# Optimization experiments

Hardware: AMD Instinct MI355X
Metric: run time of the kernel (lower is better)

Reference implementation:

```python
import jax, jax.numpy as jnp
import numpy as np

B, C, H, W = 16, 96, 96, 96
K, N, R, CR = 4, 8, 6, 12  # scan dirs, d_state, dt_rank, SE hidden


def channel_ln(x, g, b, eps=1e-6):
    # LayerNorm over channel dim (channel_first)
    mu = jnp.mean(x, axis=1, keepdims=True)
    var = jnp.var(x, axis=1, keepdims=True)
    return (x - mu) * jax.lax.rsqrt(var + eps) * g[None, :, None, None] + b[None, :, None, None]


def conv1x1(x, w, b):
    return jnp.einsum('bchw,dc->bdhw', x, w) + b[None, :, None, None]


def ss2d(x, xproj_w, dtproj_w, dtproj_b, A_logs, Ds, g, bta):
    # 4-direction selective scan (VMamba SS2D core). x: (B,C,H,W)
    Bq, Cq, Hq, Wq = x.shape
    L = Hq * Wq
    xf = x.reshape(Bq, Cq, L)
    xt = jnp.transpose(x, (0, 1, 3, 2)).reshape(Bq, Cq, L)
    xs = jnp.stack([xf, xt, xf[..., ::-1], xt[..., ::-1]], axis=1)  # (B,K,C,L)
    x_dbl = jnp.einsum('bkcl,kdc->bkdl', xs, xproj_w)  # (B,K,R+2N,L)
    dts, Bs, Cs = jnp.split(x_dbl, [R, R + N], axis=2)
    delta = jax.nn.softplus(jnp.einsum('bkrl,kcr->bkcl', dts, dtproj_w) + dtproj_b[None, :, :, None])
    A = -jnp.exp(A_logs)  # (K,C,N)
    u_t = jnp.moveaxis(xs, -1, 0)   # (L,B,K,C)
    d_t = jnp.moveaxis(delta, -1, 0)
    B_t = jnp.moveaxis(Bs, -1, 0)   # (L,B,K,N)
    C_t = jnp.moveaxis(Cs, -1, 0)
    h0 = jnp.zeros((Bq, K, Cq, N), x.dtype)

    @jax.checkpoint
    def step(h, inp):
        u, d, Bv, Cv = inp
        dA = jnp.exp(d[..., None] * A)                      # (B,K,C,N)
        h = dA * h + (d * u)[..., None] * Bv[:, :, None, :]
        return h, jnp.sum(h * Cv[:, :, None, :], axis=-1)   # (B,K,C)

    _, ys = jax.lax.scan(step, h0, (u_t, d_t, B_t, C_t))
    ys = jnp.moveaxis(ys, 0, -1) + Ds[None, :, :, None] * xs  # (B,K,C,L)

    def untrans(yk):
        return jnp.transpose(yk.reshape(Bq, Cq, Wq, Hq), (0, 1, 3, 2)).reshape(Bq, Cq, L)

    out = ys[:, 0] + untrans(ys[:, 1]) + ys[:, 2, :, ::-1] + untrans(ys[:, 3][..., ::-1])
    return channel_ln(out.reshape(Bq, Cq, Hq, Wq), g, bta)


def block_forward(x, ln_g, ln_b, p1_w, p1_b, p2in_w, p2in_b, dw_w, dw_b,
                  xproj_w, dtproj_w, dtproj_b, A_logs, Ds, ssln_g, ssln_b,
                  p2n_g, p2n_b, ca_w1, ca_b1, ca_w2, ca_b2, block_idx):
    h = channel_ln(x, ln_g, ln_b)
    a = jax.nn.silu(conv1x1(h, p1_w, p1_b))
    z = conv1x1(h, p2in_w, p2in_b)
    z = jax.lax.conv_general_dilated(z, dw_w, (1, 1), 'SAME',
                                     dimension_numbers=('NCHW', 'OIHW', 'NCHW'),
                                     feature_group_count=z.shape[1]) + dw_b[None, :, None, None]
    z = jax.nn.silu(z)
    if block_idx % 2 == 0:
        z = jnp.transpose(z, (0, 1, 3, 2))
    else:
        z = z[:, :, ::-1, ::-1]
    z = ss2d(z, xproj_w, dtproj_w, dtproj_b, A_logs, Ds, ssln_g, ssln_b)
    if block_idx % 2 == 0:
        z = jnp.transpose(z, (0, 1, 3, 2))
    else:
        z = z[:, :, ::-1, ::-1]
    z = channel_ln(z, p2n_g, p2n_b)
    y = a * z
    # channel attention (SE)
    s = jnp.mean(y, axis=(2, 3))  # (B,C)
    att = jax.nn.sigmoid(jnp.einsum('cr,br->bc', ca_w2,
                                    jax.nn.silu(jnp.einsum('rc,bc->br', ca_w1, s) + ca_b1)) + ca_b2)
    return x + y * att[:, :, None, None]


def local_mamba(x, params, block_idx):
    b, c, h, w = x.shape
    h2, w2 = h // 2, w // 2
    qs = jnp.stack([x[:, :, :h2, :w2], x[:, :, :h2, w2:],
                    x[:, :, h2:, :w2], x[:, :, h2:, w2:]])  # (4,B,C,h2,w2)
    fn = lambda q, *p: block_forward(q, *p, block_idx)
    outs = jax.vmap(fn)(qs, *params)
    top = jnp.concatenate([outs[0], outs[1]], axis=3)
    bot = jnp.concatenate([outs[2], outs[3]], axis=3)
    return jnp.concatenate([top, bot], axis=2)


def setup_inputs() -> dict:
    key = jax.random.key(0)
    ks = jax.random.split(key, 12)
    rn = lambda k, shape, s=1.0: jax.random.normal(k, shape, jnp.float32) * s
    return dict(
        x=rn(ks[0], (B, C, H, W)),
        ln_g=jnp.ones((4, C)), ln_b=jnp.zeros((4, C)),
        p1_w=rn(ks[1], (4, C, C), C ** -0.5), p1_b=jnp.zeros((4, C)),
        p2in_w=rn(ks[2], (4, C, C), C ** -0.5), p2in_b=jnp.zeros((4, C)),
        dw_w=rn(ks[3], (4, C, 1, 3, 3), 1.0 / 3.0), dw_b=jnp.zeros((4, C)),
        xproj_w=rn(ks[4], (4, K, R + 2 * N, C), C ** -0.5),
        dtproj_w=rn(ks[5], (4, K, C, R), R ** -0.5),
        dtproj_b=rn(ks[6], (4, K, C), 0.1),
        A_logs=jax.random.uniform(ks[7], (4, K, C, N), jnp.float32, 0.0, 1.0),
        Ds=jnp.ones((4, K, C)),
        ssln_g=jnp.ones((4, C)), ssln_b=jnp.zeros((4, C)),
        p2n_g=jnp.ones((4, C)), p2n_b=jnp.zeros((4, C)),
        ca_w1=rn(ks[8], (4, CR, C), C ** -0.5), ca_b1=jnp.zeros((4, CR)),
        ca_w2=rn(ks[9], (4, C, CR), CR ** -0.5), ca_b2=jnp.zeros((4, C)),
        block_idx=0,
    )


def reference(x, ln_g, ln_b, p1_w, p1_b, p2in_w, p2in_b, dw_w, dw_b,
              xproj_w, dtproj_w, dtproj_b, A_logs, Ds, ssln_g, ssln_b,
              p2n_g, p2n_b, ca_w1, ca_b1, ca_w2, ca_b2, block_idx):
    params = (ln_g, ln_b, p1_w, p1_b, p2in_w, p2in_b, dw_w, dw_b,
              xproj_w, dtproj_w, dtproj_b, A_logs, Ds, ssln_g, ssln_b,
              p2n_g, p2n_b, ca_w1, ca_b1, ca_w2, ca_b2)
    return local_mamba(x, params, block_idx)
```

## Files before the change

kernel.cpp:

```cpp
#include <hip/hip_runtime.h>
#include <hip/hip_bf16.h>

#define BQ 16
#define CN 96
#define HQ 48
#define LL 2304
#define NK 4
#define RR 6
#define NNS 8
#define DPJ 22
#define CRr 12
#define LOG2E 1.4426950408889634f

using bf16 = __hip_bfloat16;

typedef __attribute__((ext_vector_type(8))) short bf16x8;
typedef __attribute__((ext_vector_type(4))) float f32x4;

__device__ __forceinline__ float b2f(bf16 v) { return __bfloat162float(v); }
__device__ __forceinline__ bf16  f2b(float v){ return __float2bfloat16(v); }
__device__ __forceinline__ float bflo(unsigned u){ return __uint_as_float(u << 16); }
__device__ __forceinline__ float bfhi(unsigned u){ return __uint_as_float(u & 0xffff0000u); }
__device__ __forceinline__ float sigf(float x){ return 1.f / (1.f + __expf(-x)); }
__device__ __forceinline__ float siluf(float x){ return x / (1.f + __expf(-x)); }
__device__ __forceinline__ unsigned packbf(float a, float b){
    unsigned lo = (unsigned)__builtin_bit_cast(unsigned short, f2b(a));
    unsigned hi = (unsigned)__builtin_bit_cast(unsigned short, f2b(b));
    return lo | (hi << 16);
}
__device__ __forceinline__ unsigned rot16(unsigned u){ return (u >> 16) | (u << 16); }
__device__ __forceinline__ void unpack8(uint4 v, float* f){
    f[0]=bflo(v.x); f[1]=bfhi(v.x); f[2]=bflo(v.y); f[3]=bfhi(v.y);
    f[4]=bflo(v.z); f[5]=bfhi(v.z); f[6]=bflo(v.w); f[7]=bfhi(v.w);
}
__device__ __forceinline__ void unpack4(uint2 v, float* f){
    f[0]=bflo(v.x); f[1]=bfhi(v.x); f[2]=bflo(v.y); f[3]=bfhi(v.y);
}
__device__ __forceinline__ float fexp2(float x){
#if __has_builtin(__builtin_amdgcn_exp2f)
    return __builtin_amdgcn_exp2f(x);
#else
    return __expf(x * 0.6931471805599453f);
#endif
}
__device__ __forceinline__ float qxor(float v, int ctrl_b1){
    int x;
    if (ctrl_b1) x = __builtin_amdgcn_mov_dpp(__float_as_int(v), 0xB1, 0xF, 0xF, true);
    else         x = __builtin_amdgcn_mov_dpp(__float_as_int(v), 0x4E, 0xF, 0xF, true);
    return __int_as_float(x);
}

__global__ __launch_bounds__(192) void k_lnconv(
    const float* __restrict__ x, const float* __restrict__ ln_g, const float* __restrict__ ln_b,
    const float* __restrict__ p1w, const float* __restrict__ p1b,
    const float* __restrict__ p2w, const float* __restrict__ p2b,
    bf16* __restrict__ a_out, bf16* __restrict__ z0_out)
{
    const int hh2 = blockIdx.x;
    const int b = blockIdx.y, q = blockIdx.z;
    const int h0 = (q >> 1) * HQ, w0 = (q & 1) * HQ;
    const int tid = threadIdx.x;
    const int qb = q * BQ + b;

    __shared__ alignas(16) bf16 wl2[192 * 104];
    __shared__ alignas(16) bf16 hn2[96 * 104];
    __shared__ float mu[96], rs[96];
    __shared__ float pmu[192], pv2[192];
    __shared__ float biasLds[192];
    __shared__ float gl[96], bl[96];

    for (int t = tid; t < 192 * 24; t += 192) {
        int row = t / 24, c4 = (t % 24) * 4;
        const float* srcw = (row < 96) ? &p1w[(q * CN + row) * CN + c4]
                                       : &p2w[(q * CN + (row - 96)) * CN + c4];
        float4 wv = *reinterpret_cast<const float4*>(srcw);
        uint2 pk; pk.x = packbf(wv.x, wv.y); pk.y = packbf(wv.z, wv.w);
        *reinterpret_cast<uint2*>(&wl2[row * 104 + c4]) = pk;
    }
    if (tid < 192)
        biasLds[tid] = (tid < 96) ? p1b[q * CN + tid] : p2b[q * CN + (tid - 96)];
    if (tid < 96) { gl[tid] = ln_g[q * CN + tid]; bl[tid] = ln_b[q * CN + tid]; }
    for (int t = tid; t < CN * 24; t += 192) {
        int c = t / 24, v = t % 24;
        int row = v / 12, col = (v % 12) * 4;
        int p = row * 48 + col;
        float4 xv = *reinterpret_cast<const float4*>(
            &x[((b * CN + c) * 96 + h0 + 2 * hh2 + row) * 96 + w0 + col]);
        hn2[p * 104 + c]       = f2b(xv.x);
        hn2[(p + 1) * 104 + c] = f2b(xv.y);
        hn2[(p + 2) * 104 + c] = f2b(xv.z);
        hn2[(p + 3) * 104 + c] = f2b(xv.w);
    }
    __syncthreads();
    {
        int p = tid % 96, half = tid / 96;
        const bf16* hp = &hn2[p * 104 + half * 48];
        float s = 0.f, s2 = 0.f;
        #pragma unroll
        for (int c8 = 0; c8 < 48; c8 += 8) {
            float f[8]; unpack8(*reinterpret_cast<const uint4*>(hp + c8), f);
            #pragma unroll
            for (int i = 0; i < 8; ++i) { s += f[i]; s2 += f[i] * f[i]; }
        }
        pmu[half * 96 + p] = s; pv2[half * 96 + p] = s2;
    }
    __syncthreads();
    if (tid < 96) {
        float s = pmu[tid] + pmu[96 + tid];
        float s2 = pv2[tid] + pv2[96 + tid];
        float m = s * (1.f / 96.f);
        float var = s2 * (1.f / 96.f) - m * m;
        mu[tid] = m; rs[tid] = rsqrtf(var + 1e-6f);
    }
    __syncthreads();
    for (int t = tid; t < 96 * 12; t += 192) {
        int p = t / 12, c8 = (t % 12) * 8;
        float f[8]; unpack8(*reinterpret_cast<const uint4*>(&hn2[p * 104 + c8]), f);
        float m = mu[p], r = rs[p];
        unsigned ou[4];
        #pragma unroll
        for (int i = 0; i < 8; i += 2) {
            float v0 = (f[i]     - m) * r * gl[c8 + i]     + bl[c8 + i];
            float v1 = (f[i + 1] - m) * r * gl[c8 + i + 1] + bl[c8 + i + 1];
            ou[i >> 1] = packbf(v0, v1);
        }
        uint4 ov; ov.x = ou[0]; ov.y = ou[1]; ov.z = ou[2]; ov.w = ou[3];
        *reinterpret_cast<uint4*>(&hn2[p * 104 + c8]) = ov;
    }
    __syncthreads();
    const int w = tid >> 6;
    const int l = tid & 63;
    const int lr = l & 15;
    const int lq = l >> 4;
    f32x4 acc[4][6];
    #pragma unroll
    for (int m = 0; m < 4; ++m)
        #pragma unroll
        for (int n = 0; n < 6; ++n)
            acc[m][n] = (f32x4){0.f, 0.f, 0.f, 0.f};
    #pragma unroll
    for (int k0 = 0; k0 < 96; k0 += 32) {
        bf16x8 afr[4], bfr[6];
        #pragma unroll
        for (int m = 0; m < 4; ++m)
            afr[m] = *reinterpret_cast<const bf16x8*>(
                &wl2[(w * 64 + m * 16 + lr) * 104 + k0 + lq * 8]);
        #pragma unroll
        for (int n = 0; n < 6; ++n)
            bfr[n] = *reinterpret_cast<const bf16x8*>(
                &hn2[(n * 16 + lr) * 104 + k0 + lq * 8]);
        #pragma unroll
        for (int m = 0; m < 4; ++m)
            #pragma unroll
            for (int n = 0; n < 6; ++n)
                acc[m][n] = __builtin_amdgcn_mfma_f32_16x16x32_bf16(
                    afr[m], bfr[n], acc[m][n], 0, 0, 0);
    }
    #pragma unroll
    for (int m = 0; m < 4; ++m) {
        const int Rbase = w * 64 + m * 16 + lq * 4;
        #pragma unroll
        for (int n = 0; n < 6; ++n) {
            const int col = n * 16 + lr;
            const int colin = (col >= 48) ? (col - 48) : col;
            const int lbase = (2 * hh2 + (col >= 48 ? 1 : 0)) * 48 + colin;
            #pragma unroll
            for (int r = 0; r < 4; ++r) {
                const int R = Rbase + r;
                const bool isA = R < 96;
                const int d = isA ? R : R - 96;
                float v = acc[m][n][r] + biasLds[R];
                if (isA) v = siluf(v);
                bf16* dst = isA ? a_out : z0_out;
                dst[(size_t)(qb * CN + d) * LL + lbase] = f2b(v);
            }
        }
    }
}

__global__ __launch_bounds__(256) void k_dwconv(
    const bf16* __restrict__ z0, const float* __restrict__ dww, const float* __restrict__ dwb,
    const int* __restrict__ bidx, bf16* __restrict__ zt, bf16* __restrict__ ztT)
{
    const int c = blockIdx.x, b = blockIdx.y, q = blockIdx.z;
    const int tid = threadIdx.x;
    const int base = ((q * BQ + b) * CN + c) * LL;
    __shared__ float zin[50 * 50];
    __shared__ float zo[48 * 49];
    if (tid < 196) {
        int idx;
        if (tid < 50)       idx = tid;
        else if (tid < 100) idx = 49 * 50 + (tid - 50);
        else if (tid < 148) idx = (tid - 99) * 50;
        else                idx = (tid - 147) * 50 + 49;
        zin[idx] = 0.f;
    }
    for (int t = tid; t < 288; t += 256) {
        uint4 v = *reinterpret_cast<const uint4*>(&z0[base + t * 8]);
        float f[8]; unpack8(v, f);
        int e0 = t * 8, row = e0 / 48, col = e0 % 48;
        float* dst = &zin[(row + 1) * 50 + col + 1];
        #pragma unroll
        for (int i = 0; i < 8; ++i) dst[i] = f[i];
    }
    float wk[9];
    #pragma unroll
    for (int i = 0; i < 9; ++i) wk[i] = dww[(q * CN + c) * 9 + i];
    const float bias = dwb[q * CN + c];
    __syncthreads();
    for (int t = tid; t < LL; t += 256) {
        int hh = t / 48, ww = t % 48;
        const float* z0r = &zin[hh * 50 + ww];
        float s = bias;
        s = fmaf(wk[0], z0r[0],        s);
        s = fmaf(wk[1], z0r[1],        s);
        s = fmaf(wk[2], z0r[2],        s);
        s = fmaf(wk[3], z0r[50],       s);
        s = fmaf(wk[4], z0r[51],       s);
        s = fmaf(wk[5], z0r[52],       s);
        s = fmaf(wk[6], z0r[100],      s);
        s = fmaf(wk[7], z0r[101],      s);
        s = fmaf(wk[8], z0r[102],      s);
        zo[hh * 49 + ww] = siluf(s);
    }
    __syncthreads();
    const bool even = ((bidx[0] & 1) == 0);
    for (int idx = tid; idx < 288; idx += 256) {
        int e0 = idx * 8, i = e0 / 48, j = e0 % 48;
        float vz[8], vzT[8];
        if (even) {
            #pragma unroll
            for (int m = 0; m < 8; ++m) { vz[m] = zo[(j + m) * 49 + i];  vzT[m] = zo[i * 49 + j + m]; }
        } else {
            #pragma unroll
            for (int m = 0; m < 8; ++m) { vz[m] = zo[(47 - i) * 49 + (47 - j - m)];
                                          vzT[m] = zo[(47 - j - m) * 49 + (47 - i)]; }
        }
        uint4 oa, ob;
        oa.x = packbf(vz[0], vz[1]);   oa.y = packbf(vz[2], vz[3]);
        oa.z = packbf(vz[4], vz[5]);   oa.w = packbf(vz[6], vz[7]);
        ob.x = packbf(vzT[0], vzT[1]); ob.y = packbf(vzT[2], vzT[3]);
        ob.z = packbf(vzT[4], vzT[5]); ob.w = packbf(vzT[6], vzT[7]);
        *reinterpret_cast<uint4*>(&zt[base + e0])  = oa;
        *reinterpret_cast<uint4*>(&ztT[base + e0]) = ob;
    }
}

__global__ __launch_bounds__(192) void k_xdbl(
    const bf16* __restrict__ zt, const bf16* __restrict__ ztT,
    const float* __restrict__ xprojw, bf16* __restrict__ xdbl)
{
    const int lt = blockIdx.x, k = blockIdx.y, qb = blockIdx.z;
    const int tid = threadIdx.x;
    const int l0 = lt * 96;
    const int q = qb >> 4;
    __shared__ alignas(16) bf16 wl3[32 * 104];
    __shared__ alignas(16) bf16 tmp[96 * 104];
    __shared__ alignas(16) bf16 ub[96 * 104];
    const bf16* __restrict__ src = (k & 1) ? ztT : zt;
    const bool rev = (k >= 2);

    for (int t = tid; t < 520; t += 192)
        reinterpret_cast<unsigned*>(&wl3[22 * 104])[t] = 0u;
    for (int t = tid; t < DPJ * 24; t += 192) {
        int d = t / 24, c4 = (t % 24) * 4;
        float4 wv = *reinterpret_cast<const float4*>(
            &xprojw[((q * NK + k) * DPJ + d) * CN + c4]);
        uint2 pk; pk.x = packbf(wv.x, wv.y); pk.y = packbf(wv.z, wv.w);
        *reinterpret_cast<uint2*>(&wl3[d * 104 + c4]) = pk;
    }
    for (int t = tid; t < CN * 12; t += 192) {
        int cc = t / 12, j0 = (t % 12) * 8;
        uint4 v;
        if (!rev) {
            v = *reinterpret_cast<const uint4*>(&src[(size_t)(qb * CN + cc) * LL + l0 + j0]);
        } else {
            v = *reinterpret_cast<const uint4*>(&src[(size_t)(qb * CN + cc) * LL + (LL - (l0 + j0) - 8)]);
            uint4 r; r.x = rot16(v.w); r.y = rot16(v.z); r.z = rot16(v.y); r.w = rot16(v.x);
            v = r;
        }
        *reinterpret_cast<uint4*>(&tmp[cc * 104 + j0]) = v;
    }
    __syncthreads();
    for (int t = tid; t < 96 * 12; t += 192) {
        int ll = t % 96, c0 = (t / 96) * 8;
        const unsigned short* ts = reinterpret_cast<const unsigned short*>(tmp);
        unsigned e[8];
        #pragma unroll
        for (int i = 0; i < 8; ++i) e[i] = ts[(c0 + i) * 104 + ll];
        uint4 v;
        v.x = e[0] | (e[1] << 16); v.y = e[2] | (e[3] << 16);
        v.z = e[4] | (e[5] << 16); v.w = e[6] | (e[7] << 16);
        *reinterpret_cast<uint4*>(&ub[ll * 104 + c0]) = v;
    }
    __syncthreads();
    const int w = tid >> 6;
    const int ln = tid & 63;
    const int lr = ln & 15;
    const int lq = ln >> 4;
    f32x4 acc[2][2];
    #pragma unroll
    for (int m = 0; m < 2; ++m)
        #pragma unroll
        for (int n = 0; n < 2; ++n)
            acc[m][n] = (f32x4){0.f, 0.f, 0.f, 0.f};
    #pragma unroll
    for (int k0 = 0; k0 < 96; k0 += 32) {
        bf16x8 afr[2], bfr[2];
        #pragma unroll
        for (int m = 0; m < 2; ++m)
            afr[m] = *reinterpret_cast<const bf16x8*>(
                &wl3[(m * 16 + lr) * 104 + k0 + lq * 8]);
        #pragma unroll
        for (int n = 0; n < 2; ++n)
            bfr[n] = *reinterpret_cast<const bf16x8*>(
                &ub[((2 * w + n) * 16 + lr) * 104 + k0 + lq * 8]);
        #pragma unroll
        for (int m = 0; m < 2; ++m)
            #pragma unroll
            for (int n = 0; n < 2; ++n)
                acc[m][n] = __builtin_amdgcn_mfma_f32_16x16x32_bf16(
                    afr[m], bfr[n], acc[m][n], 0, 0, 0);
    }
    const size_t obase = (size_t)(qb * NK + k) * (DPJ * LL);
    #pragma unroll
    for (int m = 0; m < 2; ++m) {
        #pragma unroll
        for (int n = 0; n < 2; ++n) {
            const int lpos = l0 + (2 * w + n) * 16 + lr;
            #pragma unroll
            for (int r = 0; r < 4; ++r) {
                const int d = m * 16 + lq * 4 + r;
                if (d < DPJ)
                    xdbl[obase + (size_t)d * LL + lpos] = f2b(acc[m][n][r]);
            }
        }
    }
}


#define SCAN_BARRIER() asm volatile("s_waitcnt lgkmcnt(0)\n\ts_barrier" ::: "memory")

#define UWORD(NUA, IDX) (((IDX) & 3) == 0 ? NUA[(IDX) >> 2].x : \
                         ((IDX) & 3) == 1 ? NUA[(IDX) >> 2].y : \
                         ((IDX) & 3) == 2 ? NUA[(IDX) >> 2].z : NUA[(IDX) >> 2].w)

#define ROT3(v) (v) = ((v) == 2) ? 0 : ((v) + 1)

__global__ __launch_bounds__(384) void k_scan(
    const bf16* __restrict__ zt, const bf16* __restrict__ ztT,
    const bf16* __restrict__ xdbl,
    const float* __restrict__ dtw_g, const float* __restrict__ dtb_g,
    const float* __restrict__ Alog_g, const float* __restrict__ Ds_g,
    bf16* __restrict__ ys)
{
    const int bid = blockIdx.x;
    const int ch2 = bid & 1, k = (bid >> 1) & 3, qb = bid >> 3, q = qb >> 4;
    const int qk = q * NK + k;
    const int tid = threadIdx.x;
    const bool isScan = (tid < 192);
    const int lt = isScan ? tid : (tid - 192);
    const int ca = lt >> 2, p = lt & 3;
    const int c = ch2 * 48 + ca;

    __shared__ float dd3[3][48 * 52];
    __shared__ float xr3[3][6 * 52];
    __shared__ float bcv3[3][48 * 16];

    const bf16* __restrict__ src = (k & 1) ? ztT : zt;
    const bool rev = (k >= 2);
    const int ja = p * 12;

    float wdt[6] = {0.f, 0.f, 0.f, 0.f, 0.f, 0.f};
    float dtbc = 0.f;
    if (!isScan) {
        const float* wp = dtw_g + (size_t)qk * CN * RR + c * RR;
        float2 wa = *reinterpret_cast<const float2*>(wp);
        float2 wb = *reinterpret_cast<const float2*>(wp + 2);
        float2 wc = *reinterpret_cast<const float2*>(wp + 4);
        wdt[0] = wa.x; wdt[1] = wa.y; wdt[2] = wb.x; wdt[3] = wb.y; wdt[4] = wc.x; wdt[5] = wc.y;
        dtbc = dtb_g[qk * CN + c];
    }
    const bool xload = (!isScan) && (lt < 132);
    const int vr = lt / 6, jx = (lt % 6) * 8;
    const bf16* gx = xdbl + (size_t)(qb * NK + k) * (DPJ * LL) + (size_t)vr * LL + jx;
    int bccol = 0;
    if (vr >= 6) {
        int v = vr - 6;
        int n = v & 7;
        bccol = (n >> 1) * 4 + ((v >= 8) ? 2 : 0) + (n & 1);
    }

    float A0L = 0.f, A1L = 0.f, Dc = 0.f;
    if (isScan) {
        A0L = -__expf(Alog_g[((size_t)qk * CN + c) * NNS + 2 * p])     * LOG2E;
        A1L = -__expf(Alog_g[((size_t)qk * CN + c) * NNS + 2 * p + 1]) * LOG2E;
        Dc = Ds_g[qk * CN + c];
    }
    float h0 = 0.f, h1 = 0.f;
    const bf16* gu = src + (size_t)(qb * CN + c) * LL + (rev ? (LL - 48) : 0);
    const int ustep = rev ? -48 : 48;
    bf16* yp = ys + (size_t)(qb * NK + k) * (CN * LL) + (size_t)c * LL;

    #define COMMIT_BLOCK(PXV, XRB, BCB) do {                                          \
        if (xload) {                                                                  \
            float g[8]; unpack8(PXV, g);                                              \
            if (vr < 6) {                                                             \
                *reinterpret_cast<float4*>(&(XRB)[vr * 52 + jx])                      \
                    = make_float4(g[0], g[1], g[2], g[3]);                            \
                *reinterpret_cast<float4*>(&(XRB)[vr * 52 + jx + 4])                  \
                    = make_float4(g[4], g[5], g[6], g[7]);                            \
            } else {                                                                  \
                _Pragma("unroll")                                                     \
                for (int i = 0; i < 8; ++i) (BCB)[(jx + i) * 16 + bccol] = g[i];      \
            }                                                                         \
        }                                                                             \
    } while (0)

    #define DELTA_BLOCK(XRB, DDB) do {                                                \
        float acc[12];                                                                \
        _Pragma("unroll")                                                             \
        for (int i = 0; i < 12; ++i) acc[i] = dtbc;                                   \
        _Pragma("unroll")                                                             \
        for (int r = 0; r < 6; ++r) {                                                 \
            float4 d0 = *reinterpret_cast<const float4*>(&(XRB)[r * 52 + ja]);        \
            float4 d1 = *reinterpret_cast<const float4*>(&(XRB)[r * 52 + ja + 4]);    \
            float4 d2 = *reinterpret_cast<const float4*>(&(XRB)[r * 52 + ja + 8]);    \
            float wr_ = wdt[r];                                                       \
            acc[0] = fmaf(wr_, d0.x, acc[0]);  acc[1] = fmaf(wr_, d0.y, acc[1]);      \
            acc[2] = fmaf(wr_, d0.z, acc[2]);  acc[3] = fmaf(wr_, d0.w, acc[3]);      \
            acc[4] = fmaf(wr_, d1.x, acc[4]);  acc[5] = fmaf(wr_, d1.y, acc[5]);      \
            acc[6] = fmaf(wr_, d1.z, acc[6]);  acc[7] = fmaf(wr_, d1.w, acc[7]);      \
            acc[8] = fmaf(wr_, d2.x, acc[8]);  acc[9] = fmaf(wr_, d2.y, acc[9]);      \
            acc[10] = fmaf(wr_, d2.z, acc[10]); acc[11] = fmaf(wr_, d2.w, acc[11]);   \
        }                                                                             \
        _Pragma("unroll")                                                             \
        for (int i = 0; i < 12; ++i) {                                                \
            float a = acc[i];                                                         \
            acc[i] = (a > 15.f) ? a : __logf(1.f + __expf(a));                        \
        }                                                                             \
        float4* dp = reinterpret_cast<float4*>(&(DDB)[ca * 52 + ja]);                 \
        dp[0] = make_float4(acc[0], acc[1], acc[2], acc[3]);                          \
        dp[1] = make_float4(acc[4], acc[5], acc[6], acc[7]);                          \
        dp[2] = make_float4(acc[8], acc[9], acc[10], acc[11]);                        \
    } while (0)

    uint4 u_a[6], u_b[6];
    uint4 px_a = {0,0,0,0}, px_b = {0,0,0,0}, px1 = {0,0,0,0};
    if (isScan) {
        #pragma unroll
        for (int i = 0; i < 6; ++i) u_a[i] = *reinterpret_cast<const uint4*>(gu + i * 8);
        gu += ustep;
        #pragma unroll
        for (int i = 0; i < 6; ++i) u_b[i] = *reinterpret_cast<const uint4*>(gu + i * 8);
        gu += ustep;
    } else {
        uint4 px0 = {0,0,0,0};
        if (xload) {
            px0  = *reinterpret_cast<const uint4*>(gx);
            px1  = *reinterpret_cast<const uint4*>(gx + 48);
            px_a = *reinterpret_cast<const uint4*>(gx + 96);
            px_b = *reinterpret_cast<const uint4*>(gx + 144);
            gx += 192;
        }
        COMMIT_BLOCK(px0, xr3[0], bcv3[0]);
    }
    SCAN_BARRIER();
    if (!isScan) {
        DELTA_BLOCK(xr3[0], dd3[0]);
        COMMIT_BLOCK(px1, xr3[1], bcv3[1]);
    }
    SCAN_BARRIER();

    int s_cur = 0;
    int d_idx = 1, c_idx = 2;

    #define PROD_BODY(CH, PX) do {                                                    \
        const int chp_ = (CH);                                                        \
        if (chp_ + 2 < 48) COMMIT_BLOCK(PX, xr3[c_idx], bcv3[c_idx]);                 \
        if (chp_ + 4 < 48 && xload) { PX = *reinterpret_cast<const uint4*>(gx); gx += 48; } \
        if (chp_ + 1 < 48) DELTA_BLOCK(xr3[d_idx], dd3[d_idx]);                       \
        ROT3(d_idx); ROT3(c_idx);                                                     \
    } while (0)

    #define SCAN_CHUNK(CH, UC) do {                                                   \
        const int ch_ = (CH);                                                         \
        uint4 nu[6];                                                                  \
        if (!rev) {                                                                   \
            nu[0] = UC[0]; nu[1] = UC[1]; nu[2] = UC[2];                              \
            nu[3] = UC[3]; nu[4] = UC[4]; nu[5] = UC[5];                              \
        } else {                                                                      \
            _Pragma("unroll")                                                         \
            for (int qq = 0; qq < 6; ++qq) {                                          \
                nu[qq].x = rot16(UC[5 - qq].w); nu[qq].y = rot16(UC[5 - qq].z);       \
                nu[qq].z = rot16(UC[5 - qq].y); nu[qq].w = rot16(UC[5 - qq].x);       \
            }                                                                         \
        }                                                                             \
        {                                                                             \
            const int l0 = ch_ * 48;                                                  \
            const float* ddc = &dd3[s_cur][ca * 52];                                  \
            const float* bcc = &bcv3[s_cur][p * 4];                                   \
            _Pragma("unroll")                                                         \
            for (int gg = 0; gg < 6; ++gg) {                                          \
                unsigned pk[4];                                                       \
                _Pragma("unroll")                                                     \
                for (int half = 0; half < 2; ++half) {                                \
                    const int j0 = gg * 8 + half * 4;                                 \
                    float4 d4 = *reinterpret_cast<const float4*>(ddc + j0);           \
                    const float* df = reinterpret_cast<const float*>(&d4);            \
                    _Pragma("unroll")                                                 \
                    for (int s = 0; s < 4; ++s) {                                     \
                        const int j = j0 + s;                                         \
                        const unsigned uwv = UWORD(nu, j >> 1);                       \
                        float u = (j & 1) ? bfhi(uwv) : bflo(uwv);                    \
                        float d = df[s];                                              \
                        float4 bq = *reinterpret_cast<const float4*>(bcc + j * 16);   \
                        float du = d * u;                                             \
                        float dA0 = fexp2(d * A0L);                                   \
                        float dA1 = fexp2(d * A1L);                                   \
                        h0 = fmaf(dA0, h0, du * bq.x);                                \
                        h1 = fmaf(dA1, h1, du * bq.y);                                \
                        float y = fmaf(h0, bq.z, h1 * bq.w);                          \
                        y += qxor(y, 1); y += qxor(y, 0);                             \
                        y = fmaf(Dc, u, y);                                           \
                        unsigned hb = (unsigned)__builtin_bit_cast(unsigned short, f2b(y)); \
                        const int sl = half * 4 + s;                                  \
                        if (sl & 1) pk[sl >> 1] |= hb << 16; else pk[sl >> 1] = hb;   \
                    }                                                                 \
                }                                                                     \
                if (p == 0) {                                                         \
                    uint4 wv4; wv4.x = pk[0]; wv4.y = pk[1]; wv4.z = pk[2]; wv4.w = pk[3]; \
                    *reinterpret_cast<uint4*>(yp + l0 + gg * 8) = wv4;                \
                }                                                                     \
            }                                                                         \
        }                                                                             \
        if (ch_ + 2 < 48) {                                                           \
            _Pragma("unroll")                                                         \
            for (int i = 0; i < 6; ++i) UC[i] = *reinterpret_cast<const uint4*>(gu + i * 8); \
            gu += ustep;                                                              \
        }                                                                             \
        ROT3(s_cur);                                                                  \
    } while (0)

    for (int t = 0; t < 24; ++t) {
        if (isScan) SCAN_CHUNK(2 * t, u_a);
        else        PROD_BODY(2 * t, px_a);
        SCAN_BARRIER();
        if (isScan) SCAN_CHUNK(2 * t + 1, u_b);
        else        PROD_BODY(2 * t + 1, px_b);
        SCAN_BARRIER();
    }

    #undef SCAN_CHUNK
    #undef PROD_BODY
    #undef DELTA_BLOCK
    #undef COMMIT_BLOCK
}

__global__ __launch_bounds__(256) void k_sum(
    const bf16* __restrict__ ys, bf16* __restrict__ s_out)
{
    const int c = blockIdx.x, b = blockIdx.y, q = blockIdx.z;
    const int qb = q * BQ + b;
    const int tid = threadIdx.x;
    __shared__ float t0[48 * 49];
    __shared__ float t2[48 * 49];
    const size_t base0 = ((size_t)(qb * NK + 0) * CN + c) * LL;
    const size_t base1 = ((size_t)(qb * NK + 1) * CN + c) * LL;
    const size_t base2 = ((size_t)(qb * NK + 2) * CN + c) * LL;
    const size_t base3 = ((size_t)(qb * NK + 3) * CN + c) * LL;
    for (int idx = tid; idx < 288; idx += 256) {
        int e0 = idx * 8, h = e0 / 48, w = e0 % 48;
        float f[8];
        unpack8(*reinterpret_cast<const uint4*>(&ys[base0 + e0]), f);
        #pragma unroll
        for (int i = 0; i < 8; ++i) t0[h * 49 + w + i] = f[i];
        unpack8(*reinterpret_cast<const uint4*>(&ys[base2 + e0]), f);
        #pragma unroll
        for (int i = 0; i < 8; ++i) t2[h * 49 + w + i] = f[i];
    }
    __syncthreads();
    const size_t cbase = ((size_t)qb * CN + c) * LL;
    for (int idx = tid; idx < 288; idx += 256) {
        int m0 = idx * 8, ww = m0 / 48, hh = m0 % 48;
        float f1[8], f3[8];
        unpack8(*reinterpret_cast<const uint4*>(&ys[base1 + m0]), f1);
        unpack8(*reinterpret_cast<const uint4*>(&ys[base3 + (LL - 8 - m0)]), f3);
        float o[8];
        #pragma unroll
        for (int i = 0; i < 8; ++i) {
            float v0 = t0[(hh + i) * 49 + ww];
            float v2 = t2[(47 - hh - i) * 49 + (47 - ww)];
            o[i] = v0 + f1[i] + v2 + f3[7 - i];
        }
        uint4 w;
        w.x = packbf(o[0], o[1]); w.y = packbf(o[2], o[3]);
        w.z = packbf(o[4], o[5]); w.w = packbf(o[6], o[7]);
        *reinterpret_cast<uint4*>(&s_out[cbase + m0]) = w;
    }
}

__global__ __launch_bounds__(256) void k_combine(
    const bf16* __restrict__ s_in, const bf16* __restrict__ a_in,
    const float* __restrict__ ssg, const float* __restrict__ ssb,
    const float* __restrict__ png, const float* __restrict__ pnb,
    const int* __restrict__ bidx,
    bf16* __restrict__ y_out, float* __restrict__ s_buf)
{
    const int ww = blockIdx.x, b = blockIdx.y, q = blockIdx.z;
    const int qb = q * BQ + b;
    const int tid = threadIdx.x;
    __shared__ float o[CN * 48];
    __shared__ float mu[48], rs[48];
    __shared__ float pp[192], pp2[192];
    for (int v = tid; v < 576; v += 256) {
        int e0 = v * 8, cc = e0 / 48, hh = e0 % 48;
        float f[8];
        unpack8(*reinterpret_cast<const uint4*>(&s_in[((size_t)qb * CN + cc) * LL + ww * 48 + hh]), f);
        #pragma unroll
        for (int i = 0; i < 8; ++i) o[cc * 48 + hh + i] = f[i];
    }
    __syncthreads();
    if (tid < 192) {
        int hh = tid % 48, part = tid / 48;
        float s = 0.f, s2 = 0.f;
        int c0 = part * 24;
        for (int cc = c0; cc < c0 + 24; ++cc) { float v = o[cc * 48 + hh]; s += v; s2 += v * v; }
        pp[tid] = s; pp2[tid] = s2;
    }
    __syncthreads();
    if (tid < 48) {
        float s = pp[tid] + pp[tid + 48] + pp[tid + 96] + pp[tid + 144];
        float s2 = pp2[tid] + pp2[tid + 48] + pp2[tid + 96] + pp2[tid + 144];
        float m = s * (1.f / 96.f), var = s2 * (1.f / 96.f) - m * m;
        mu[tid] = m; rs[tid] = rsqrtf(var + 1e-6f);
    }
    __syncthreads();
    for (int t = tid; t < CN * 48; t += 256) {
        int cc = t / 48, hh = t % 48;
        o[t] = (o[t] - mu[hh]) * rs[hh] * ssg[q * CN + cc] + ssb[q * CN + cc];
    }
    __syncthreads();
    if (tid < 192) {
        int hh = tid % 48, part = tid / 48;
        float s = 0.f, s2 = 0.f;
        int c0 = part * 24;
        for (int cc = c0; cc < c0 + 24; ++cc) { float v = o[cc * 48 + hh]; s += v; s2 += v * v; }
        pp[tid] = s; pp2[tid] = s2;
    }
    __syncthreads();
    if (tid < 48) {
        float s = pp[tid] + pp[tid + 48] + pp[tid + 96] + pp[tid + 144];
        float s2 = pp2[tid] + pp2[tid + 48] + pp2[tid + 96] + pp2[tid + 144];
        float m = s * (1.f / 96.f), var = s2 * (1.f / 96.f) - m * m;
        mu[tid] = m; rs[tid] = rsqrtf(var + 1e-6f);
    }
    __syncthreads();
    const bool even = ((bidx[0] & 1) == 0);
    if (even) {
        for (int v = tid; v < 576; v += 256) {
            int e0 = v * 8, cc = e0 / 48, hh = e0 % 48;
            size_t oidx = ((size_t)qb * CN + cc) * LL + ww * 48 + hh;
            float af[8];
            unpack8(*reinterpret_cast<const uint4*>(&a_in[oidx]), af);
            float yv[8];
            #pragma unroll
            for (int i = 0; i < 8; ++i) {
                float z2 = (o[cc * 48 + hh + i] - mu[hh + i]) * rs[hh + i] * png[q * CN + cc] + pnb[q * CN + cc];
                yv[i] = af[i] * z2;
                o[cc * 48 + hh + i] = yv[i];
            }
            uint4 w;
            w.x = packbf(yv[0], yv[1]); w.y = packbf(yv[2], yv[3]);
            w.z = packbf(yv[4], yv[5]); w.w = packbf(yv[6], yv[7]);
            *reinterpret_cast<uint4*>(&y_out[oidx]) = w;
        }
    } else {
        for (int t = tid; t < CN * 48; t += 256) {
            int cc = t / 48, hh = t % 48;
            float z2 = (o[t] - mu[hh]) * rs[hh] * png[q * CN + cc] + pnb[q * CN + cc];
            size_t oidx = ((size_t)qb * CN + cc) * LL + (47 - hh) * 48 + (47 - ww);
            float yv = b2f(a_in[oidx]) * z2;
            y_out[oidx] = f2b(yv);
            o[t] = yv;
        }
    }
    __syncthreads();
    if (tid < CN) {
        float s = 0.f;
        for (int j = 0; j < 48; ++j) s += o[tid * 48 + j];
        atomicAdd(&s_buf[qb * CN + tid], s);
    }
}

__global__ __launch_bounds__(256) void k_final(
    const float* __restrict__ x, const bf16* __restrict__ y_in,
    const float* __restrict__ s_buf,
    const float* __restrict__ w1, const float* __restrict__ b1,
    const float* __restrict__ w2, const float* __restrict__ b2,
    float* __restrict__ out)
{
    const int c = blockIdx.x, b = blockIdx.y, q = blockIdx.z;
    const int h0 = (q >> 1) * HQ, w0 = (q & 1) * HQ;
    const int qb = q * BQ + b;
    const int tid = threadIdx.x;
    __shared__ float tl[CRr];
    __shared__ float tpart[16 * CRr];
    __shared__ float attv;
    if (tid < 192) {
        int r = tid % CRr, part = tid / CRr;
        float acc = 0.f;
        const float* wr = w1 + (q * CRr + r) * CN;
        const float* sb = s_buf + qb * CN;
        int c0 = part * 6;
        for (int cc = c0; cc < c0 + 6; ++cc)
            acc = fmaf(wr[cc], sb[cc] * (1.f / (float)LL), acc);
        tpart[part * CRr + r] = acc;
    }
    __syncthreads();
    if (tid < CRr) {
        float acc = b1[q * CRr + tid];
        #pragma unroll
        for (int pt = 0; pt < 16; ++pt) acc += tpart[pt * CRr + tid];
        tl[tid] = siluf(acc);
    }
    __syncthreads();
    if (tid == 0) {
        float acc = b2[q * CN + c];
        #pragma unroll
        for (int r = 0; r < CRr; ++r) acc = fmaf(w2[(q * CN + c) * CRr + r], tl[r], acc);
        attv = sigf(acc);
    }
    __syncthreads();
    const float av = attv;
    const size_t ybase = (size_t)(qb * CN + c) * LL;
    const int xb = (b * CN + c) * 9216 + h0 * 96 + w0;
    for (int t = tid; t < LL / 8; t += 256) {
        int e0 = t * 8;
        int gi = xb + (e0 / 48) * 96 + (e0 % 48);
        uint4 yv = *reinterpret_cast<const uint4*>(&y_in[ybase + e0]);
        float yf[8]; unpack8(yv, yf);
        float4 xa = *reinterpret_cast<const float4*>(&x[gi]);
        float4 xc = *reinterpret_cast<const float4*>(&x[gi + 4]);
        float4 o0 = {xa.x + yf[0]*av, xa.y + yf[1]*av, xa.z + yf[2]*av, xa.w + yf[3]*av};
        float4 o1 = {xc.x + yf[4]*av, xc.y + yf[5]*av, xc.z + yf[6]*av, xc.w + yf[7]*av};
        *reinterpret_cast<float4*>(&out[gi])     = o0;
        *reinterpret_cast<float4*>(&out[gi + 4]) = o1;
    }
}

extern "C" void kernel_launch(void* const* d_in, const int* in_sizes, int n_in,
                              void* d_out, int out_size, void* d_ws, size_t ws_size,
                              hipStream_t stream)
{
    (void)in_sizes; (void)n_in; (void)out_size; (void)ws_size;
    const float* x       = (const float*)d_in[0];
    const float* ln_g    = (const float*)d_in[1];
    const float* ln_b    = (const float*)d_in[2];
    const float* p1_w    = (const float*)d_in[3];
    const float* p1_b    = (const float*)d_in[4];
    const float* p2in_w  = (const float*)d_in[5];
    const float* p2in_b  = (const float*)d_in[6];
    const float* dw_w    = (const float*)d_in[7];
    const float* dw_b    = (const float*)d_in[8];
    const float* xproj_w = (const float*)d_in[9];
    const float* dtproj_w= (const float*)d_in[10];
    const float* dtproj_b= (const float*)d_in[11];
    const float* A_logs  = (const float*)d_in[12];
    const float* Ds      = (const float*)d_in[13];
    const float* ssln_g  = (const float*)d_in[14];
    const float* ssln_b  = (const float*)d_in[15];
    const float* p2n_g   = (const float*)d_in[16];
    const float* p2n_b   = (const float*)d_in[17];
    const float* ca_w1   = (const float*)d_in[18];
    const float* ca_b1   = (const float*)d_in[19];
    const float* ca_w2   = (const float*)d_in[20];
    const float* ca_b2   = (const float*)d_in[21];
    const int*  bidx     = (const int*)d_in[22];
    float* out = (float*)d_out;

    char* ws = (char*)d_ws;
    const size_t off_a    = 0;
    const size_t off_zt   = 28311552;
    const size_t off_ztT  = 56623104;
    const size_t off_xdbl = 84934656;
    const size_t off_ys   = 110886912;
    const size_t off_z0   = off_ys;
    const size_t off_s    = off_zt;
    const size_t off_y    = off_ztT;
    const size_t off_sb   = 224133120;

    bf16*  a_buf   = (bf16*)(ws + off_a);
    bf16*  zt_buf  = (bf16*)(ws + off_zt);
    bf16*  ztT_buf = (bf16*)(ws + off_ztT);
    bf16*  xdbl_buf= (bf16*)(ws + off_xdbl);
    bf16*  ys_buf  = (bf16*)(ws + off_ys);
    bf16*  z0_buf  = (bf16*)(ws + off_z0);
    bf16*  s_sum   = (bf16*)(ws + off_s);
    bf16*  y_buf   = (bf16*)(ws + off_y);
    float* s_buf   = (float*)(ws + off_sb);

    (void)hipMemsetAsync(ws + off_sb, 0, 24576, stream);

    k_lnconv<<<dim3(24, 16, 4), 192, 0, stream>>>(
        x, ln_g, ln_b, p1_w, p1_b, p2in_w, p2in_b, a_buf, z0_buf);
    k_dwconv<<<dim3(96, 16, 4), 256, 0, stream>>>(
        z0_buf, dw_w, dw_b, bidx, zt_buf, ztT_buf);
    k_xdbl<<<dim3(24, 4, 64), 192, 0, stream>>>(
        zt_buf, ztT_buf, xproj_w, xdbl_buf);
    k_scan<<<dim3(512), 384, 0, stream>>>(
        zt_buf, ztT_buf, xdbl_buf, dtproj_w, dtproj_b, A_logs, Ds, ys_buf);
    k_sum<<<dim3(96, 16, 4), 256, 0, stream>>>(
        ys_buf, s_sum);
    k_combine<<<dim3(48, 16, 4), 256, 0, stream>>>(
        s_sum, a_buf, ssln_g, ssln_b, p2n_g, p2n_b, bidx, y_buf, s_buf);
    k_final<<<dim3(96, 16, 4), 256, 0, stream>>>(
        x, y_buf, s_buf, ca_w1, ca_b1, ca_w2, ca_b2, out);
}
```

Measured before the change: 604.8 us.

## Split selective scan into segmented three-pass scan with carry propagation

Replaces the single sequential scan kernel with a chunked parallel scan. The first pass computes per-segment state and decay products over 12 segments. A small kernel prefix-combines the carries, and the final pass rescans each segment from its carried-in state and writes outputs. This exposes far more blocks than the original 512-block launch to hide the serial-latency bound. In exchange it reads the inputs twice, recomputes delta and exp in both passes, and needs extra workspace, so it falls back to the old kernel when the workspace is too small.

```diff
diff --git a/kernel.cpp b/kernel.cpp
--- a/kernel.cpp
+++ b/kernel.cpp
@@ -212,15 +212,15 @@
         int hh = t / 48, ww = t % 48;
         const float* z0r = &zin[hh * 50 + ww];
         float s = bias;
-        s = fmaf(wk[0], z0r[0],        s);
-        s = fmaf(wk[1], z0r[1],        s);
-        s = fmaf(wk[2], z0r[2],        s);
-        s = fmaf(wk[3], z0r[50],       s);
-        s = fmaf(wk[4], z0r[51],       s);
-        s = fmaf(wk[5], z0r[52],       s);
-        s = fmaf(wk[6], z0r[100],      s);
-        s = fmaf(wk[7], z0r[101],      s);
-        s = fmaf(wk[8], z0r[102],      s);
+        s = fmaf(wk[0], z0r[0],   s);
+        s = fmaf(wk[1], z0r[1],   s);
+        s = fmaf(wk[2], z0r[2],   s);
+        s = fmaf(wk[3], z0r[50],  s);
+        s = fmaf(wk[4], z0r[51],  s);
+        s = fmaf(wk[5], z0r[52],  s);
+        s = fmaf(wk[6], z0r[100], s);
+        s = fmaf(wk[7], z0r[101], s);
+        s = fmaf(wk[8], z0r[102], s);
         zo[hh * 49 + ww] = siluf(s);
     }
     __syncthreads();
@@ -557,6 +557,310 @@
     #undef COMMIT_BLOCK
 }
 
+#define SEGCH 4
+#define NSEG 12
+
+__global__ __launch_bounds__(192) void k_scanA(
+    const bf16* __restrict__ zt, const bf16* __restrict__ ztT,
+    const bf16* __restrict__ xdbl,
+    const float* __restrict__ dtw_g, const float* __restrict__ dtb_g,
+    const float* __restrict__ Alog_g,
+    float4* __restrict__ carry)
+{
+    const int bid = blockIdx.x;
+    const int seg = bid % NSEG, rest = bid / NSEG;
+    const int ch2 = rest & 1, k = (rest >> 1) & 3, qb = rest >> 3, q = qb >> 4;
+    const int qk = q * NK + k;
+    const int lt = threadIdx.x;
+    const int ca = lt >> 2, p = lt & 3;
+    const int c = ch2 * 48 + ca;
+
+    __shared__ float dd[48 * 52];
+    __shared__ float xr[6 * 52];
+    __shared__ float bcv[48 * 16];
+
+    const float* wp = dtw_g + (size_t)qk * CN * RR + c * RR;
+    float wdt[6];
+    {
+        float2 wa = *reinterpret_cast<const float2*>(wp);
+        float2 wb = *reinterpret_cast<const float2*>(wp + 2);
+        float2 wc = *reinterpret_cast<const float2*>(wp + 4);
+        wdt[0] = wa.x; wdt[1] = wa.y; wdt[2] = wb.x; wdt[3] = wb.y; wdt[4] = wc.x; wdt[5] = wc.y;
+    }
+    const float dtbc = dtb_g[qk * CN + c];
+    const float A0L = -__expf(Alog_g[((size_t)qk * CN + c) * NNS + 2 * p])     * LOG2E;
+    const float A1L = -__expf(Alog_g[((size_t)qk * CN + c) * NNS + 2 * p + 1]) * LOG2E;
+    const bf16* __restrict__ src = (k & 1) ? ztT : zt;
+    const bool rev = (k >= 2);
+    const int ja = p * 12;
+    const bool xload = (lt < 132);
+    const int vr = lt / 6, jx = (lt % 6) * 8;
+    int bccol = 0;
+    if (vr >= 6) {
+        int v = vr - 6;
+        int n = v & 7;
+        bccol = (n >> 1) * 4 + ((v >= 8) ? 2 : 0) + (n & 1);
+    }
+    const size_t xb = (size_t)(qb * NK + k) * (DPJ * LL);
+    const size_t ubase = (size_t)(qb * CN + c) * LL;
+
+    float h0 = 0.f, h1 = 0.f, a0 = 1.f, a1 = 1.f;
+
+    for (int ch = 0; ch < SEGCH; ++ch) {
+        const int g = seg * SEGCH + ch;
+        uint4 uu[6];
+        {
+            const bf16* gu = src + ubase + (rev ? (LL - 48 - 48 * g) : 48 * g);
+            #pragma unroll
+            for (int i = 0; i < 6; ++i) uu[i] = *reinterpret_cast<const uint4*>(gu + i * 8);
+        }
+        uint4 px = {0,0,0,0};
+        if (xload) px = *reinterpret_cast<const uint4*>(&xdbl[xb + (size_t)vr * LL + g * 48 + jx]);
+        __syncthreads();
+        if (xload) {
+            float gv[8]; unpack8(px, gv);
+            if (vr < 6) {
+                *reinterpret_cast<float4*>(&xr[vr * 52 + jx])     = make_float4(gv[0], gv[1], gv[2], gv[3]);
+                *reinterpret_cast<float4*>(&xr[vr * 52 + jx + 4]) = make_float4(gv[4], gv[5], gv[6], gv[7]);
+            } else {
+                #pragma unroll
+                for (int i = 0; i < 8; ++i) bcv[(jx + i) * 16 + bccol] = gv[i];
+            }
+        }
+        __syncthreads();
+        {
+            float acc[12];
+            #pragma unroll
+            for (int i = 0; i < 12; ++i) acc[i] = dtbc;
+            #pragma unroll
+            for (int r = 0; r < 6; ++r) {
+                float4 d0 = *reinterpret_cast<const float4*>(&xr[r * 52 + ja]);
+                float4 d1 = *reinterpret_cast<const float4*>(&xr[r * 52 + ja + 4]);
+                float4 d2 = *reinterpret_cast<const float4*>(&xr[r * 52 + ja + 8]);
+                float wr_ = wdt[r];
+                acc[0] = fmaf(wr_, d0.x, acc[0]);  acc[1] = fmaf(wr_, d0.y, acc[1]);
+                acc[2] = fmaf(wr_, d0.z, acc[2]);  acc[3] = fmaf(wr_, d0.w, acc[3]);
+                acc[4] = fmaf(wr_, d1.x, acc[4]);  acc[5] = fmaf(wr_, d1.y, acc[5]);
+                acc[6] = fmaf(wr_, d1.z, acc[6]);  acc[7] = fmaf(wr_, d1.w, acc[7]);
+                acc[8] = fmaf(wr_, d2.x, acc[8]);  acc[9] = fmaf(wr_, d2.y, acc[9]);
+                acc[10] = fmaf(wr_, d2.z, acc[10]); acc[11] = fmaf(wr_, d2.w, acc[11]);
+            }
+            #pragma unroll
+            for (int i = 0; i < 12; ++i) {
+                float a = acc[i];
+                acc[i] = (a > 15.f) ? a : __logf(1.f + __expf(a));
+            }
+            float4* dp = reinterpret_cast<float4*>(&dd[ca * 52 + ja]);
+            dp[0] = make_float4(acc[0], acc[1], acc[2], acc[3]);
+            dp[1] = make_float4(acc[4], acc[5], acc[6], acc[7]);
+            dp[2] = make_float4(acc[8], acc[9], acc[10], acc[11]);
+        }
+        __syncthreads();
+        uint4 nu[6];
+        if (!rev) {
+            nu[0] = uu[0]; nu[1] = uu[1]; nu[2] = uu[2];
+            nu[3] = uu[3]; nu[4] = uu[4]; nu[5] = uu[5];
+        } else {
+            #pragma unroll
+            for (int qq = 0; qq < 6; ++qq) {
+                nu[qq].x = rot16(uu[5 - qq].w); nu[qq].y = rot16(uu[5 - qq].z);
+                nu[qq].z = rot16(uu[5 - qq].y); nu[qq].w = rot16(uu[5 - qq].x);
+            }
+        }
+        const float* ddc = &dd[ca * 52];
+        const float* bcc = &bcv[p * 4];
+        #pragma unroll
+        for (int gg = 0; gg < 6; ++gg) {
+            #pragma unroll
+            for (int half = 0; half < 2; ++half) {
+                const int j0 = gg * 8 + half * 4;
+                float4 d4 = *reinterpret_cast<const float4*>(ddc + j0);
+                const float* df = reinterpret_cast<const float*>(&d4);
+                #pragma unroll
+                for (int s = 0; s < 4; ++s) {
+                    const int j = j0 + s;
+                    const unsigned uwv = UWORD(nu, j >> 1);
+                    float u = (j & 1) ? bfhi(uwv) : bflo(uwv);
+                    float d = df[s];
+                    float4 bq = *reinterpret_cast<const float4*>(bcc + j * 16);
+                    float du = d * u;
+                    float dA0 = fexp2(d * A0L);
+                    float dA1 = fexp2(d * A1L);
+                    h0 = fmaf(dA0, h0, du * bq.x);
+                    h1 = fmaf(dA1, h1, du * bq.y);
+                    a0 *= dA0; a1 *= dA1;
+                }
+            }
+        }
+    }
+    carry[(size_t)bid * 192 + lt] = make_float4(h0, h1, a0, a1);
+}
+
+__global__ __launch_bounds__(192) void k_scanB(float4* __restrict__ carry)
+{
+    const int bid = blockIdx.x;
+    const int lt = threadIdx.x;
+    float hi0 = 0.f, hi1 = 0.f;
+    for (int seg = 0; seg < NSEG; ++seg) {
+        const size_t idx = ((size_t)(bid * NSEG + seg)) * 192 + lt;
+        float4 cr = carry[idx];
+        carry[idx] = make_float4(hi0, hi1, 0.f, 0.f);
+        hi0 = fmaf(cr.z, hi0, cr.x);
+        hi1 = fmaf(cr.w, hi1, cr.y);
+    }
+}
+
+__global__ __launch_bounds__(192) void k_scanC(
+    const bf16* __restrict__ zt, const bf16* __restrict__ ztT,
+    const bf16* __restrict__ xdbl,
+    const float* __restrict__ dtw_g, const float* __restrict__ dtb_g,
+    const float* __restrict__ Alog_g, const float* __restrict__ Ds_g,
+    const float4* __restrict__ carry,
+    bf16* __restrict__ ys)
+{
+    const int bid = blockIdx.x;
+    const int seg = bid % NSEG, rest = bid / NSEG;
+    const int ch2 = rest & 1, k = (rest >> 1) & 3, qb = rest >> 3, q = qb >> 4;
+    const int qk = q * NK + k;
+    const int lt = threadIdx.x;
+    const int ca = lt >> 2, p = lt & 3;
+    const int c = ch2 * 48 + ca;
+
+    __shared__ float dd[48 * 52];
+    __shared__ float xr[6 * 52];
+    __shared__ float bcv[48 * 16];
+
+    const float* wp = dtw_g + (size_t)qk * CN * RR + c * RR;
+    float wdt[6];
+    {
+        float2 wa = *reinterpret_cast<const float2*>(wp);
+        float2 wb = *reinterpret_cast<const float2*>(wp + 2);
+        float2 wc = *reinterpret_cast<const float2*>(wp + 4);
+        wdt[0] = wa.x; wdt[1] = wa.y; wdt[2] = wb.x; wdt[3] = wb.y; wdt[4] = wc.x; wdt[5] = wc.y;
+    }
+    const float dtbc = dtb_g[qk * CN + c];
+    const float A0L = -__expf(Alog_g[((size_t)qk * CN + c) * NNS + 2 * p])     * LOG2E;
+    const float A1L = -__expf(Alog_g[((size_t)qk * CN + c) * NNS + 2 * p + 1]) * LOG2E;
+    const float Dc = Ds_g[qk * CN + c];
+    const bf16* __restrict__ src = (k & 1) ? ztT : zt;
+    const bool rev = (k >= 2);
+    const int ja = p * 12;
+    const bool xload = (lt < 132);
+    const int vr = lt / 6, jx = (lt % 6) * 8;
+    int bccol = 0;
+    if (vr >= 6) {
+        int v = vr - 6;
+        int n = v & 7;
+        bccol = (n >> 1) * 4 + ((v >= 8) ? 2 : 0) + (n & 1);
+    }
+    const size_t xb = (size_t)(qb * NK + k) * (DPJ * LL);
+    const size_t ubase = (size_t)(qb * CN + c) * LL;
+    bf16* yp = ys + (size_t)(qb * NK + k) * (CN * LL) + (size_t)c * LL;
+
+    float4 cr = carry[(size_t)bid * 192 + lt];
+    float h0 = cr.x, h1 = cr.y;
+
+    for (int ch = 0; ch < SEGCH; ++ch) {
+        const int g = seg * SEGCH + ch;
+        uint4 uu[6];
+        {
+            const bf16* gu = src + ubase + (rev ? (LL - 48 - 48 * g) : 48 * g);
+            #pragma unroll
+            for (int i = 0; i < 6; ++i) uu[i] = *reinterpret_cast<const uint4*>(gu + i * 8);
+        }
+        uint4 px = {0,0,0,0};
+        if (xload) px = *reinterpret_cast<const uint4*>(&xdbl[xb + (size_t)vr * LL + g * 48 + jx]);
+        __syncthreads();
+        if (xload) {
+            float gv[8]; unpack8(px, gv);
+            if (vr < 6) {
+                *reinterpret_cast<float4*>(&xr[vr * 52 + jx])     = make_float4(gv[0], gv[1], gv[2], gv[3]);
+                *reinterpret_cast<float4*>(&xr[vr * 52 + jx + 4]) = make_float4(gv[4], gv[5], gv[6], gv[7]);
+            } else {
+                #pragma unroll
+                for (int i = 0; i < 8; ++i) bcv[(jx + i) * 16 + bccol] = gv[i];
+            }
+        }
+        __syncthreads();
+        {
+            float acc[12];
+            #pragma unroll
+            for (int i = 0; i < 12; ++i) acc[i] = dtbc;
+            #pragma unroll
+            for (int r = 0; r < 6; ++r) {
+                float4 d0 = *reinterpret_cast<const float4*>(&xr[r * 52 + ja]);
+                float4 d1 = *reinterpret_cast<const float4*>(&xr[r * 52 + ja + 4]);
+                float4 d2 = *reinterpret_cast<const float4*>(&xr[r * 52 + ja + 8]);
+                float wr_ = wdt[r];
+                acc[0] = fmaf(wr_, d0.x, acc[0]);  acc[1] = fmaf(wr_, d0.y, acc[1]);
+                acc[2] = fmaf(wr_, d0.z, acc[2]);  acc[3] = fmaf(wr_, d0.w, acc[3]);
+                acc[4] = fmaf(wr_, d1.x, acc[4]);  acc[5] = fmaf(wr_, d1.y, acc[5]);
+                acc[6] = fmaf(wr_, d1.z, acc[6]);  acc[7] = fmaf(wr_, d1.w, acc[7]);
+                acc[8] = fmaf(wr_, d2.x, acc[8]);  acc[9] = fmaf(wr_, d2.y, acc[9]);
+                acc[10] = fmaf(wr_, d2.z, acc[10]); acc[11] = fmaf(wr_, d2.w, acc[11]);
+            }
+            #pragma unroll
+            for (int i = 0; i < 12; ++i) {
+                float a = acc[i];
+                acc[i] = (a > 15.f) ? a : __logf(1.f + __expf(a));
+            }
+            float4* dp = reinterpret_cast<float4*>(&dd[ca * 52 + ja]);
+            dp[0] = make_float4(acc[0], acc[1], acc[2], acc[3]);
+            dp[1] = make_float4(acc[4], acc[5], acc[6], acc[7]);
+            dp[2] = make_float4(acc[8], acc[9], acc[10], acc[11]);
+        }
+        __syncthreads();
+        uint4 nu[6];
+        if (!rev) {
+            nu[0] = uu[0]; nu[1] = uu[1]; nu[2] = uu[2];
+            nu[3] = uu[3]; nu[4] = uu[4]; nu[5] = uu[5];
+        } else {
+            #pragma unroll
+            for (int qq = 0; qq < 6; ++qq) {
+                nu[qq].x = rot16(uu[5 - qq].w); nu[qq].y = rot16(uu[5 - qq].z);
+                nu[qq].z = rot16(uu[5 - qq].y); nu[qq].w = rot16(uu[5 - qq].x);
+            }
+        }
+        const int l0 = g * 48;
+        const float* ddc = &dd[ca * 52];
+        const float* bcc = &bcv[p * 4];
+        #pragma unroll
+        for (int gg = 0; gg < 6; ++gg) {
+            unsigned pk[4];
+            #pragma unroll
+            for (int half = 0; half < 2; ++half) {
+                const int j0 = gg * 8 + half * 4;
+                float4 d4 = *reinterpret_cast<const float4*>(ddc + j0);
+                const float* df = reinterpret_cast<const float*>(&d4);
+                #pragma unroll
+                for (int s = 0; s < 4; ++s) {
+                    const int j = j0 + s;
+                    const unsigned uwv = UWORD(nu, j >> 1);
+                    float u = (j & 1) ? bfhi(uwv) : bflo(uwv);
+                    float d = df[s];
+                    float4 bq = *reinterpret_cast<const float4*>(bcc + j * 16);
+                    float du = d * u;
+                    float dA0 = fexp2(d * A0L);
+                    float dA1 = fexp2(d * A1L);
+                    h0 = fmaf(dA0, h0, du * bq.x);
+                    h1 = fmaf(dA1, h1, du * bq.y);
+                    float y = fmaf(h0, bq.z, h1 * bq.w);
+                    y += qxor(y, 1); y += qxor(y, 0);
+                    y = fmaf(Dc, u, y);
+                    unsigned hb = (unsigned)__builtin_bit_cast(unsigned short, f2b(y));
+                    const int sl = half * 4 + s;
+                    if (sl & 1) pk[sl >> 1] |= hb << 16; else pk[sl >> 1] = hb;
+                }
+            }
+            if (p == 0) {
+                uint4 wv4; wv4.x = pk[0]; wv4.y = pk[1]; wv4.z = pk[2]; wv4.w = pk[3];
+                *reinterpret_cast<uint4*>(yp + l0 + gg * 8) = wv4;
+            }
+        }
+        __syncthreads();
+    }
+}
+
 __global__ __launch_bounds__(256) void k_sum(
     const bf16* __restrict__ ys, bf16* __restrict__ s_out)
 {
@@ -753,7 +1057,7 @@
                               void* d_out, int out_size, void* d_ws, size_t ws_size,
                               hipStream_t stream)
 {
-    (void)in_sizes; (void)n_in; (void)out_size; (void)ws_size;
+    (void)in_sizes; (void)n_in; (void)out_size;
     const float* x       = (const float*)d_in[0];
     const float* ln_g    = (const float*)d_in[1];
     const float* ln_b    = (const float*)d_in[2];
@@ -789,6 +1093,9 @@
     const size_t off_s    = off_zt;
     const size_t off_y    = off_ztT;
     const size_t off_sb   = 224133120;
+    const size_t off_cr   = 224157696;
+    const size_t cr_bytes = (size_t)6144 * 192 * 16;
+    const size_t need_cp  = off_cr + cr_bytes;
 
     bf16*  a_buf   = (bf16*)(ws + off_a);
     bf16*  zt_buf  = (bf16*)(ws + off_zt);
@@ -799,6 +1106,7 @@
     bf16*  s_sum   = (bf16*)(ws + off_s);
     bf16*  y_buf   = (bf16*)(ws + off_y);
     float* s_buf   = (float*)(ws + off_sb);
+    float4* carry  = (float4*)(ws + off_cr);
 
     (void)hipMemsetAsync(ws + off_sb, 0, 24576, stream);
 
@@ -808,8 +1116,16 @@
         z0_buf, dw_w, dw_b, bidx, zt_buf, ztT_buf);
     k_xdbl<<<dim3(24, 4, 64), 192, 0, stream>>>(
         zt_buf, ztT_buf, xproj_w, xdbl_buf);
-    k_scan<<<dim3(512), 384, 0, stream>>>(
-        zt_buf, ztT_buf, xdbl_buf, dtproj_w, dtproj_b, A_logs, Ds, ys_buf);
+    if (ws_size >= need_cp) {
+        k_scanA<<<dim3(6144), 192, 0, stream>>>(
+            zt_buf, ztT_buf, xdbl_buf, dtproj_w, dtproj_b, A_logs, carry);
+        k_scanB<<<dim3(512), 192, 0, stream>>>(carry);
+        k_scanC<<<dim3(6144), 192, 0, stream>>>(
+            zt_buf, ztT_buf, xdbl_buf, dtproj_w, dtproj_b, A_logs, Ds, carry, ys_buf);
+    } else {
+        k_scan<<<dim3(512), 384, 0, stream>>>(
+            zt_buf, ztT_buf, xdbl_buf, dtproj_w, dtproj_b, A_logs, Ds, ys_buf);
+    }
     k_sum<<<dim3(96, 16, 4), 256, 0, stream>>>(
         ys_buf, s_sum);
     k_combine<<<dim3(48, 16, 4), 256, 0, stream>>>(
```

Result: slower. 673.4 us (+11.3%).
